# Performance work log

Measured on AMD Instinct MI355X. Metric: run time of the kernel, lower is better.

## Reference

```python
import jax, jax.numpy as jnp
import numpy as np

# Constants matching module reset(): R_reset=5 -> R = 5+15 = 20; T = 10.0; kn=0, gn=1
G = 128          # grid_side
N = G * G        # 16384 cells
R = 20
NB = (2 * R + 3) ** 2        # 1849 = nb_neighbors per the module's assert
NSHIFT = (2 * R + 1) ** 2    # 1681 slots actually filled by the shift loop
T = 10.0
NB_RULES = 4


def _neighbor_idx():
    idx = np.arange(N)
    i, j = idx // G, idx % G
    si, sj = np.meshgrid(np.arange(-R, R + 1), np.arange(-R, R + 1), indexing='ij')
    si, sj = si.ravel(), sj.ravel()   # row-major: shift_i outer loop, shift_j inner
    nb = ((i[:, None] + si[None, :]) % G) * G + (j[:, None] + sj[None, :]) % G  # [N, NSHIFT]
    full = np.zeros((N, NB), dtype=np.int32)   # unfilled slots default to cell 0 (as in torch zeros init)
    full[:, :NSHIFT] = nb
    return jnp.asarray(full)

NEI = _neighbor_idx()   # [N, NB] int32, translation-invariant periodic neighbor list


def setup_inputs() -> dict:
    key = jax.random.key(0)
    ks = jax.random.split(key, 9)
    idx = jnp.arange(N)
    pos = jnp.stack([idx // G, idx % G], axis=-1).astype(jnp.float32)   # [N, 2] grid coords
    x = jax.random.uniform(ks[0], (N, 3), dtype=jnp.float32)            # [N, C] state in [0,1]
    c0 = jax.random.randint(ks[1], (NB_RULES,), 0, 3)                   # source channel per rule
    c1 = jax.random.randint(ks[2], (NB_RULES,), 0, 3)                   # target channel per rule
    r = 0.5 + 0.5 * jax.random.uniform(ks[3], (NB_RULES,), dtype=jnp.float32)
    rk = jax.random.uniform(ks[4], (NB_RULES, 3), dtype=jnp.float32)    # kernel ring centers
    b = jax.random.uniform(ks[5], (NB_RULES, 3), dtype=jnp.float32)     # kernel ring heights
    w = 0.1 + 0.4 * jax.random.uniform(ks[6], (NB_RULES, 3), dtype=jnp.float32)  # ring widths
    h = jax.random.uniform(ks[7], (NB_RULES,), dtype=jnp.float32)       # growth strength
    m = 0.1 + 0.4 * jax.random.uniform(ks[8], (NB_RULES,), dtype=jnp.float32)    # growth mean
    s = 0.05 + 0.1 * jax.random.uniform(jax.random.fold_in(key, 99), (NB_RULES,), dtype=jnp.float32)
    return {"pos": pos, "x": x, "c0": c0, "c1": c1, "r": r, "rk": rk,
            "b": b, "w": w, "h": h, "m": m, "s": s}


def reference(pos, x, c0, c1, r, rk, b, w, h, m, s):
    # gather neighbor states: x_ext[:, 0] is self, rest are the NB neighbors -> [N, 1+NB, C]
    x_ext = jnp.concatenate([x[:, None, :], x[NEI]], axis=1)
    # translation-invariant distance computed at the center cell (as in torch)
    center = G * G // 2 + G // 2
    dpos = jnp.concatenate([jnp.zeros((1, 2), pos.dtype), pos[NEI[center]] - pos[center]], axis=0)  # [1+NB, 2]
    dist = jnp.sqrt(jnp.sum(dpos ** 2, axis=-1)) / R   # [1+NB]
    edge_mask = jax.nn.sigmoid(-(dist - 1.0) * 10.0)
    delta_x = jnp.zeros_like(x)
    for k in range(NB_RULES):
        # kernel_core[0]: sum of Gaussian rings over the last axis
        wk = edge_mask * (b[k] * jnp.exp(-((dist[:, None] / r[k] - rk[k]) / w[k]) ** 2 / 2)).sum(-1)  # [1+NB]
        wn = wk / wk.sum()                    # per-cell weight rows are identical -> compute once
        potential = jnp.mean(wn[None, :] * x_ext[:, :, c0[k]], axis=1)   # aggr='mean' -> [N]
        # field_func[1]
        field = jnp.exp(-(potential - m[k]) ** 2 / (2 * s[k] ** 2) - 0.001) * 2 - 1
        delta_x = delta_x.at[:, c1[k]].add(h[k] * field)
    new_x = jnp.clip(x + delta_x / T, 0.0, 1.0)
    return pos, new_x
```

## Files before the change

### kernel.cpp

```cpp
#include <hip/hip_runtime.h>
#include <math.h>

#define G 128
#define NCELLS (G*G)
#define RAD 20
#define NS 41
#define NTAPS (NS*NS)
#define NB_FULL 1850.0f
#define NTAIL 168.0f
#define WROWPAD 44
#define WSZ (NS*WROWPAD)
#define NRULES 4
#define NQ 4

#define WOFF_W     0
#define WOFF_TAIL  (NRULES*WSZ)
#define WOFF_POT   (WOFF_TAIL + 4)
#define WOFF_PLANE (WOFF_POT + NRULES*NQ*NCELLS)

__device__ __forceinline__ float kernel_w(float d, float r_k,
                                          float rk0, float rk1, float rk2,
                                          float b0, float b1, float b2,
                                          float w0, float w1, float w2) {
    float em = 1.f / (1.f + expf((d - 1.f) * 10.f));
    float dd = d / r_k;
    float q0 = (dd - rk0) / w0;
    float q1 = (dd - rk1) / w1;
    float q2 = (dd - rk2) / w2;
    float ssum = b0 * expf(-0.5f * q0 * q0)
               + b1 * expf(-0.5f * q1 * q1)
               + b2 * expf(-0.5f * q2 * q2);
    return em * ssum;
}

__global__ __launch_bounds__(256)
void lenia_prep(const float* __restrict__ x,
                const float* __restrict__ rr,
                const float* __restrict__ rkv,
                const float* __restrict__ bv,
                const float* __restrict__ wv,
                float* __restrict__ ws) {
    const int bid = blockIdx.x;
    const int t = threadIdx.x;

    if (bid >= NRULES) {
        int n = (bid - NRULES) * 256 + t;
        float v0 = x[n*3 + 0];
        float v1 = x[n*3 + 1];
        float v2 = x[n*3 + 2];
        ws[WOFF_PLANE + 0*NCELLS + n] = v0;
        ws[WOFF_PLANE + 1*NCELLS + n] = v1;
        ws[WOFF_PLANE + 2*NCELLS + n] = v2;
        return;
    }

    __shared__ float red[256];
    const int k = bid;
    const float r_k = rr[k];
    const float rk0 = rkv[k*3+0], rk1 = rkv[k*3+1], rk2 = rkv[k*3+2];
    const float b0  = bv[k*3+0],  b1  = bv[k*3+1],  b2  = bv[k*3+2];
    const float w0  = wv[k*3+0],  w1  = wv[k*3+1],  w2  = wv[k*3+2];

    float vals[7];
    float lsum = 0.f;
    #pragma unroll
    for (int q = 0; q < 7; ++q) {
        int sidx = t + q * 256;
        vals[q] = 0.f;
        if (sidx < NTAPS) {
            int si = sidx / NS - RAD;
            int sj = sidx % NS - RAD;
            float d = sqrtf((float)(si*si + sj*sj)) / (float)RAD;
            float wk = kernel_w(d, r_k, rk0, rk1, rk2, b0, b1, b2, w0, w1, w2);
            vals[q] = wk;
            lsum += wk;
        }
    }
    red[t] = lsum;
    __syncthreads();
    for (int off = 128; off > 0; off >>= 1) {
        if (t < off) red[t] += red[t + off];
        __syncthreads();
    }
    const float wself = kernel_w(0.f, r_k, rk0, rk1, rk2, b0, b1, b2, w0, w1, w2);
    const float dtail = sqrtf(8192.f) / (float)RAD;
    const float wtail = kernel_w(dtail, r_k, rk0, rk1, rk2, b0, b1, b2, w0, w1, w2);
    const float S = red[0] + wself + NTAIL * wtail;
    const float inv = 1.f / (S * NB_FULL);

    #pragma unroll
    for (int q = 0; q < 7; ++q) {
        int sidx = t + q * 256;
        if (sidx < NTAPS) {
            float v = vals[q] * inv;
            if (sidx == (RAD * NS + RAD)) v += wself * inv;
            ws[WOFF_W + k*WSZ + (sidx / NS) * WROWPAD + (sidx % NS)] = v;
        }
    }
    for (int idx = t; idx < NS * (WROWPAD - NS); idx += 256) {
        int row = idx / (WROWPAD - NS);
        int col = NS + idx % (WROWPAD - NS);
        ws[WOFF_W + k*WSZ + row * WROWPAD + col] = 0.f;
    }
    if (t == 0) ws[WOFF_TAIL + k] = NTAIL * wtail * inv;
}

__global__ __launch_bounds__(256)
void lenia_conv(const int* __restrict__ c0, float* __restrict__ ws) {
    __shared__ __align__(16) float xt[14*168];

    const int bid  = blockIdx.x;
    const int q    = bid & 3;
    const int k    = (bid >> 2) & 3;
    const int tile = bid >> 4;
    const int i0   = tile * 4;
    const int t    = threadIdx.x;

    const int si0 = (q == 0) ? 0 : (q * 10 + 1);
    const int nsi = (q == 0) ? 11 : 10;
    const int r0  = i0 - RAD + si0;
    const int NR  = nsi + 3;

    const int ck = c0[k];
    const float* xp = ws + WOFF_PLANE + ck * NCELLS;
    const float* wgl = ws + WOFF_W + k * WSZ;

    for (int idx = t; idx < NR*32; idx += 256) {
        int rrow = idx >> 5, qq = idx & 31;
        int grow = (r0 + rrow) & (G - 1);
        *(float4*)&xt[rrow*168 + 20 + qq*4] = *(const float4*)&xp[grow*G + qq*4];
    }
    for (int idx = t; idx < NR*40; idx += 256) {
        int rrow = idx / 40, h = idx % 40;
        int cc = (h < 20) ? h : (h + 128);
        int grow = (r0 + rrow) & (G - 1);
        int gcol = (cc - 20) & (G - 1);
        xt[rrow*168 + cc] = xp[grow*G + gcol];
    }
    __syncthreads();

    const int row = t >> 6;
    const int colbase = (t & 63) * 2;
    float a0 = 0.f, a1 = 0.f, a2 = 0.f, a3 = 0.f;

    for (int ii = 0; ii < nsi; ++ii) {
        const float* rp = &xt[(row + ii)*168 + colbase];
        float wwin[42];
        #pragma unroll
        for (int u = 0; u < 21; ++u) {
            float2 v = *(const float2*)&rp[2*u];
            wwin[2*u] = v.x; wwin[2*u+1] = v.y;
        }
        const float* wr = wgl + (si0 + ii) * WROWPAD;
        float wrow[44];
        #pragma unroll
        for (int u = 0; u < 11; ++u) {
            float4 v = *(const float4*)&wr[4*u];
            wrow[4*u] = v.x; wrow[4*u+1] = v.y; wrow[4*u+2] = v.z; wrow[4*u+3] = v.w;
        }
        #pragma unroll
        for (int s2 = 0; s2 < 40; s2 += 2) {
            a0 = fmaf(wrow[s2],   wwin[s2],   a0);
            a1 = fmaf(wrow[s2],   wwin[s2+1], a1);
            a2 = fmaf(wrow[s2+1], wwin[s2+1], a2);
            a3 = fmaf(wrow[s2+1], wwin[s2+2], a3);
        }
        a0 = fmaf(wrow[40], wwin[40], a0);
        a1 = fmaf(wrow[40], wwin[41], a1);
    }

    int cell = (i0 + row) * G + colbase;
    float* pp = ws + WOFF_POT + (k * NQ + q) * NCELLS;
    pp[cell]     = a0 + a2;
    pp[cell + 1] = a1 + a3;
}

__global__ __launch_bounds__(256)
void lenia_update(const float* __restrict__ pos,
                  const float* __restrict__ x,
                  const int* __restrict__ c0,
                  const int* __restrict__ c1,
                  const float* __restrict__ hv,
                  const float* __restrict__ mv,
                  const float* __restrict__ sv,
                  const float* __restrict__ ws,
                  float* __restrict__ out) {
    int n = blockIdx.x * 256 + threadIdx.x;
    out[2*n]     = pos[2*n];
    out[2*n + 1] = pos[2*n + 1];

    float xv0 = x[n*3 + 0], xv1 = x[n*3 + 1], xv2 = x[n*3 + 2];
    float d0 = 0.f, d1 = 0.f, d2 = 0.f;
    #pragma unroll
    for (int k = 0; k < NRULES; ++k) {
        float tail = ws[WOFF_TAIL + k] * x[c0[k]];
        float pot = tail;
        #pragma unroll
        for (int qq = 0; qq < NQ; ++qq)
            pot += ws[WOFF_POT + (k * NQ + qq) * NCELLS + n];
        float mk = mv[k], sk = sv[k];
        float u = pot - mk;
        float field = expf(-u*u / (2.f * sk * sk) - 0.001f) * 2.f - 1.f;
        float add = hv[k] * field;
        int c = c1[k];
        if (c == 0) d0 += add; else if (c == 1) d1 += add; else d2 += add;
    }
    float* ox = out + 2*NCELLS;
    ox[n*3 + 0] = fminf(fmaxf(xv0 + d0 * 0.1f, 0.f), 1.f);
    ox[n*3 + 1] = fminf(fmaxf(xv1 + d1 * 0.1f, 0.f), 1.f);
    ox[n*3 + 2] = fminf(fmaxf(xv2 + d2 * 0.1f, 0.f), 1.f);
}

extern "C" void kernel_launch(void* const* d_in, const int* in_sizes, int n_in,
                              void* d_out, int out_size, void* d_ws, size_t ws_size,
                              hipStream_t stream) {
    const float* pos = (const float*)d_in[0];
    const float* x   = (const float*)d_in[1];
    const int*   c0  = (const int*)  d_in[2];
    const int*   c1  = (const int*)  d_in[3];
    const float* r   = (const float*)d_in[4];
    const float* rk  = (const float*)d_in[5];
    const float* b   = (const float*)d_in[6];
    const float* w   = (const float*)d_in[7];
    const float* h   = (const float*)d_in[8];
    const float* m   = (const float*)d_in[9];
    const float* s   = (const float*)d_in[10];
    float* out = (float*)d_out;
    float* ws  = (float*)d_ws;

    lenia_prep<<<NRULES + NCELLS/256, 256, 0, stream>>>(x, r, rk, b, w, ws);
    lenia_conv<<<(G/4) * NRULES * NQ, 256, 0, stream>>>(c0, ws);
    lenia_update<<<NCELLS/256, 256, 0, stream>>>(pos, x, c0, c1, h, m, s, ws, out);
}
```

Baseline: 24.71 us.

## Fuse prep, conv and update into one kernel with grid-wide atomic barrier

```diff
diff --git a/kernel.cpp b/kernel.cpp
--- a/kernel.cpp
+++ b/kernel.cpp
@@ -8,135 +8,122 @@
 #define NTAPS (NS*NS)
 #define NB_FULL 1850.0f
 #define NTAIL 168.0f
-#define WROWPAD 44
-#define WSZ (NS*WROWPAD)
 #define NRULES 4
 #define NQ 4
-
-#define WOFF_W     0
-#define WOFF_TAIL  (NRULES*WSZ)
-#define WOFF_POT   (WOFF_TAIL + 4)
-#define WOFF_PLANE (WOFF_POT + NRULES*NQ*NCELLS)
-
-__device__ __forceinline__ float kernel_w(float d, float r_k,
-                                          float rk0, float rk1, float rk2,
-                                          float b0, float b1, float b2,
-                                          float w0, float w1, float w2) {
-    float em = 1.f / (1.f + expf((d - 1.f) * 10.f));
-    float dd = d / r_k;
-    float q0 = (dd - rk0) / w0;
-    float q1 = (dd - rk1) / w1;
-    float q2 = (dd - rk2) / w2;
-    float ssum = b0 * expf(-0.5f * q0 * q0)
-               + b1 * expf(-0.5f * q1 * q1)
-               + b2 * expf(-0.5f * q2 * q2);
+#define QROWPAD 44
+#define QROWS 11
+#define QSZ (QROWS*QROWPAD)
+#define NBLOCKS 512
+#define NSLOTS 8
+
+#define WOFF_CNT  0
+#define WOFF_TAIL 128
+#define WOFF_POT  132
+#define WOFF_BW   (WOFF_POT + NRULES*NQ*NCELLS)
+
+__device__ __forceinline__ float kw(float d, float irk,
+                                    float rk0, float rk1, float rk2,
+                                    float b0, float b1, float b2,
+                                    float iw0, float iw1, float iw2) {
+    float em = 1.f / (1.f + __expf((d - 1.f) * 10.f));
+    float dd = d * irk;
+    float u0 = (dd - rk0) * iw0;
+    float u1 = (dd - rk1) * iw1;
+    float u2 = (dd - rk2) * iw2;
+    float ssum = b0 * __expf(-0.5f * u0 * u0)
+               + b1 * __expf(-0.5f * u1 * u1)
+               + b2 * __expf(-0.5f * u2 * u2);
     return em * ssum;
 }
 
-__global__ __launch_bounds__(256)
-void lenia_prep(const float* __restrict__ x,
-                const float* __restrict__ rr,
-                const float* __restrict__ rkv,
-                const float* __restrict__ bv,
-                const float* __restrict__ wv,
-                float* __restrict__ ws) {
-    const int bid = blockIdx.x;
-    const int t = threadIdx.x;
-
-    if (bid >= NRULES) {
-        int n = (bid - NRULES) * 256 + t;
-        float v0 = x[n*3 + 0];
-        float v1 = x[n*3 + 1];
-        float v2 = x[n*3 + 2];
-        ws[WOFF_PLANE + 0*NCELLS + n] = v0;
-        ws[WOFF_PLANE + 1*NCELLS + n] = v1;
-        ws[WOFF_PLANE + 2*NCELLS + n] = v2;
-        return;
-    }
-
-    __shared__ float red[256];
-    const int k = bid;
-    const float r_k = rr[k];
-    const float rk0 = rkv[k*3+0], rk1 = rkv[k*3+1], rk2 = rkv[k*3+2];
-    const float b0  = bv[k*3+0],  b1  = bv[k*3+1],  b2  = bv[k*3+2];
-    const float w0  = wv[k*3+0],  w1  = wv[k*3+1],  w2  = wv[k*3+2];
-
-    float vals[7];
-    float lsum = 0.f;
-    #pragma unroll
-    for (int q = 0; q < 7; ++q) {
-        int sidx = t + q * 256;
-        vals[q] = 0.f;
-        if (sidx < NTAPS) {
-            int si = sidx / NS - RAD;
-            int sj = sidx % NS - RAD;
-            float d = sqrtf((float)(si*si + sj*sj)) / (float)RAD;
-            float wk = kernel_w(d, r_k, rk0, rk1, rk2, b0, b1, b2, w0, w1, w2);
-            vals[q] = wk;
-            lsum += wk;
-        }
-    }
-    red[t] = lsum;
-    __syncthreads();
-    for (int off = 128; off > 0; off >>= 1) {
-        if (t < off) red[t] += red[t + off];
-        __syncthreads();
-    }
-    const float wself = kernel_w(0.f, r_k, rk0, rk1, rk2, b0, b1, b2, w0, w1, w2);
-    const float dtail = sqrtf(8192.f) / (float)RAD;
-    const float wtail = kernel_w(dtail, r_k, rk0, rk1, rk2, b0, b1, b2, w0, w1, w2);
-    const float S = red[0] + wself + NTAIL * wtail;
-    const float inv = 1.f / (S * NB_FULL);
-
-    #pragma unroll
-    for (int q = 0; q < 7; ++q) {
-        int sidx = t + q * 256;
-        if (sidx < NTAPS) {
-            float v = vals[q] * inv;
-            if (sidx == (RAD * NS + RAD)) v += wself * inv;
-            ws[WOFF_W + k*WSZ + (sidx / NS) * WROWPAD + (sidx % NS)] = v;
-        }
-    }
-    for (int idx = t; idx < NS * (WROWPAD - NS); idx += 256) {
-        int row = idx / (WROWPAD - NS);
-        int col = NS + idx % (WROWPAD - NS);
-        ws[WOFF_W + k*WSZ + row * WROWPAD + col] = 0.f;
-    }
-    if (t == 0) ws[WOFF_TAIL + k] = NTAIL * wtail * inv;
-}
-
-__global__ __launch_bounds__(256)
-void lenia_conv(const int* __restrict__ c0, float* __restrict__ ws) {
+__global__ __launch_bounds__(256, 2)
+void lenia_fused(const float* __restrict__ pos,
+                 const float* __restrict__ x,
+                 const int* __restrict__ c0v,
+                 const int* __restrict__ c1v,
+                 const float* __restrict__ rr,
+                 const float* __restrict__ rkv,
+                 const float* __restrict__ bv,
+                 const float* __restrict__ wv,
+                 const float* __restrict__ hv,
+                 const float* __restrict__ mv,
+                 const float* __restrict__ sv,
+                 float* __restrict__ ws,
+                 float* __restrict__ out) {
     __shared__ __align__(16) float xt[14*168];
+    __shared__ float red[4];
 
     const int bid  = blockIdx.x;
+    const int t    = threadIdx.x;
     const int q    = bid & 3;
     const int k    = (bid >> 2) & 3;
     const int tile = bid >> 4;
     const int i0   = tile * 4;
-    const int t    = threadIdx.x;
-
-    const int si0 = (q == 0) ? 0 : (q * 10 + 1);
-    const int nsi = (q == 0) ? 11 : 10;
-    const int r0  = i0 - RAD + si0;
-    const int NR  = nsi + 3;
-
-    const int ck = c0[k];
-    const float* xp = ws + WOFF_PLANE + ck * NCELLS;
-    const float* wgl = ws + WOFF_W + k * WSZ;
-
-    for (int idx = t; idx < NR*32; idx += 256) {
-        int rrow = idx >> 5, qq = idx & 31;
-        int grow = (r0 + rrow) & (G - 1);
-        *(float4*)&xt[rrow*168 + 20 + qq*4] = *(const float4*)&xp[grow*G + qq*4];
-    }
-    for (int idx = t; idx < NR*40; idx += 256) {
-        int rrow = idx / 40, h = idx % 40;
-        int cc = (h < 20) ? h : (h + 128);
+    const int si0  = (q == 0) ? 0 : (q * 10 + 1);
+    const int nsi  = (q == 0) ? 11 : 10;
+    const int r0   = i0 - RAD + si0;
+    const int NR   = nsi + 3;
+    const int ck   = c0v[k];
+
+    if (bid >= 64 && bid < 128) {
+        int n = (bid - 64) * 256 + t;
+        *(float2*)&out[2*n] = *(const float2*)&pos[2*n];
+    }
+
+    for (int idx = t; idx < NR * 168; idx += 256) {
+        int rrow = idx / 168;
+        int cc   = idx - rrow * 168;
         int grow = (r0 + rrow) & (G - 1);
         int gcol = (cc - 20) & (G - 1);
-        xt[rrow*168 + cc] = xp[grow*G + gcol];
-    }
+        xt[rrow*168 + cc] = x[grow*(G*3) + gcol*3 + ck];
+    }
+
+    const float irk = 1.f / rr[k];
+    const float rk0 = rkv[k*3+0], rk1 = rkv[k*3+1], rk2 = rkv[k*3+2];
+    const float b0  = bv[k*3+0],  b1  = bv[k*3+1],  b2  = bv[k*3+2];
+    const float iw0 = 1.f / wv[k*3+0], iw1 = 1.f / wv[k*3+1], iw2 = 1.f / wv[k*3+2];
+    const float invR = 1.f / (float)RAD;
+
+    float vals[7];
+    float lsum = 0.f;
+    #pragma unroll
+    for (int j = 0; j < 7; ++j) {
+        int sidx = t + j * 256;
+        float wk = 0.f;
+        if (sidx < NTAPS) {
+            int si = sidx / NS - RAD;
+            int sj = sidx % NS - RAD;
+            float d = sqrtf((float)(si*si + sj*sj)) * invR;
+            wk = kw(d, irk, rk0, rk1, rk2, b0, b1, b2, iw0, iw1, iw2);
+        }
+        vals[j] = wk;
+        lsum += wk;
+    }
+    #pragma unroll
+    for (int mm = 32; mm > 0; mm >>= 1) lsum += __shfl_xor(lsum, mm, 64);
+    if ((t & 63) == 0) red[t >> 6] = lsum;
+    __syncthreads();
+    const float S4 = red[0] + red[1] + red[2] + red[3];
+    const float wself = kw(0.f, irk, rk0, rk1, rk2, b0, b1, b2, iw0, iw1, iw2);
+    const float dtail = sqrtf(8192.f) * invR;
+    const float wtail = kw(dtail, irk, rk0, rk1, rk2, b0, b1, b2, iw0, iw1, iw2);
+    const float S = S4 + wself + NTAIL * wtail;
+    const float inv = 1.f / (S * NB_FULL);
+
+    float* bw = ws + WOFF_BW + bid * QSZ;
+    const int lo = si0 * NS, hi = (si0 + nsi) * NS;
+    #pragma unroll
+    for (int j = 0; j < 7; ++j) {
+        int sidx = t + j * 256;
+        if (sidx >= lo && sidx < hi) {
+            float v = vals[j] * inv;
+            if (sidx == RAD*NS + RAD) v += wself * inv;
+            int l = sidx - lo;
+            bw[(l / NS) * QROWPAD + (l % NS)] = v;
+        }
+    }
+    if (t < QROWS * 3) bw[(t / 3) * QROWPAD + NS + (t % 3)] = 0.f;
+    if (tile == 0 && q == 0 && t == 0) ws[WOFF_TAIL + k] = NTAIL * wtail * inv;
     __syncthreads();
 
     const int row = t >> 6;
@@ -151,7 +138,7 @@
             float2 v = *(const float2*)&rp[2*u];
             wwin[2*u] = v.x; wwin[2*u+1] = v.y;
         }
-        const float* wr = wgl + (si0 + ii) * WROWPAD;
+        const float* wr = bw + ii * QROWPAD;
         float wrow[44];
         #pragma unroll
         for (int u = 0; u < 11; ++u) {
@@ -173,42 +160,52 @@
     float* pp = ws + WOFF_POT + (k * NQ + q) * NCELLS;
     pp[cell]     = a0 + a2;
     pp[cell + 1] = a1 + a3;
-}
-
-__global__ __launch_bounds__(256)
-void lenia_update(const float* __restrict__ pos,
-                  const float* __restrict__ x,
-                  const int* __restrict__ c0,
-                  const int* __restrict__ c1,
-                  const float* __restrict__ hv,
-                  const float* __restrict__ mv,
-                  const float* __restrict__ sv,
-                  const float* __restrict__ ws,
-                  float* __restrict__ out) {
-    int n = blockIdx.x * 256 + threadIdx.x;
-    out[2*n]     = pos[2*n];
-    out[2*n + 1] = pos[2*n + 1];
-
-    float xv0 = x[n*3 + 0], xv1 = x[n*3 + 1], xv2 = x[n*3 + 2];
-    float d0 = 0.f, d1 = 0.f, d2 = 0.f;
-    #pragma unroll
-    for (int k = 0; k < NRULES; ++k) {
-        float tail = ws[WOFF_TAIL + k] * x[c0[k]];
-        float pot = tail;
-        #pragma unroll
-        for (int qq = 0; qq < NQ; ++qq)
-            pot += ws[WOFF_POT + (k * NQ + qq) * NCELLS + n];
-        float mk = mv[k], sk = sv[k];
-        float u = pot - mk;
-        float field = expf(-u*u / (2.f * sk * sk) - 0.001f) * 2.f - 1.f;
-        float add = hv[k] * field;
-        int c = c1[k];
-        if (c == 0) d0 += add; else if (c == 1) d1 += add; else d2 += add;
-    }
-    float* ox = out + 2*NCELLS;
-    ox[n*3 + 0] = fminf(fmaxf(xv0 + d0 * 0.1f, 0.f), 1.f);
-    ox[n*3 + 1] = fminf(fmaxf(xv1 + d1 * 0.1f, 0.f), 1.f);
-    ox[n*3 + 2] = fminf(fmaxf(xv2 + d2 * 0.1f, 0.f), 1.f);
+
+    __syncthreads();
+    unsigned int* cnt = (unsigned int*)ws;
+    if (t == 0) {
+        __threadfence();
+        __hip_atomic_fetch_add(&cnt[(bid & 7) * 16], 1u,
+                               __ATOMIC_ACQ_REL, __HIP_MEMORY_SCOPE_AGENT);
+    }
+    if (bid >= 64) return;
+
+    if (t == 0) {
+        unsigned int ssum;
+        do {
+            __builtin_amdgcn_s_sleep(2);
+            ssum = 0;
+            #pragma unroll
+            for (int i = 0; i < NSLOTS; ++i)
+                ssum += __hip_atomic_load(&cnt[i * 16], __ATOMIC_ACQUIRE,
+                                          __HIP_MEMORY_SCOPE_AGENT);
+        } while (ssum < NBLOCKS);
+        __threadfence();
+    }
+    __syncthreads();
+
+    {
+        int n = bid * 256 + t;
+        float xv0 = x[n*3 + 0], xv1 = x[n*3 + 1], xv2 = x[n*3 + 2];
+        float d0 = 0.f, d1 = 0.f, d2 = 0.f;
+        #pragma unroll
+        for (int kk = 0; kk < NRULES; ++kk) {
+            float pot = ws[WOFF_TAIL + kk] * x[c0v[kk]];
+            #pragma unroll
+            for (int qq = 0; qq < NQ; ++qq)
+                pot += ws[WOFF_POT + (kk * NQ + qq) * NCELLS + n];
+            float u = pot - mv[kk];
+            float sk = sv[kk];
+            float field = __expf(-u*u / (2.f * sk * sk) - 0.001f) * 2.f - 1.f;
+            float add = hv[kk] * field;
+            int c = c1v[kk];
+            if (c == 0) d0 += add; else if (c == 1) d1 += add; else d2 += add;
+        }
+        float* ox = out + 2 * NCELLS;
+        ox[n*3 + 0] = fminf(fmaxf(xv0 + d0 * 0.1f, 0.f), 1.f);
+        ox[n*3 + 1] = fminf(fmaxf(xv1 + d1 * 0.1f, 0.f), 1.f);
+        ox[n*3 + 2] = fminf(fmaxf(xv2 + d2 * 0.1f, 0.f), 1.f);
+    }
 }
 
 extern "C" void kernel_launch(void* const* d_in, const int* in_sizes, int n_in,
@@ -228,7 +225,6 @@
     float* out = (float*)d_out;
     float* ws  = (float*)d_ws;
 
-    lenia_prep<<<NRULES + NCELLS/256, 256, 0, stream>>>(x, r, rk, b, w, ws);
-    lenia_conv<<<(G/4) * NRULES * NQ, 256, 0, stream>>>(c0, ws);
-    lenia_update<<<NCELLS/256, 256, 0, stream>>>(pos, x, c0, c1, h, m, s, ws, out);
+    hipMemsetAsync(ws, 0, 512, stream);
+    lenia_fused<<<NBLOCKS, 256, 0, stream>>>(pos, x, c0, c1, r, rk, b, w, h, m, s, ws, out);
 }
```

Result: slower. 52.95 us (+114.3%).
